# Kernel optimization log

Hardware: AMD Instinct MI355X
Metric: run time of the kernel (lower is better)

## Reference

```python
import jax, jax.numpy as jnp
import numpy as np

USER_NUM = 500000
ITEM_NUM = 100000
D = 256        # embedding_size
MEM = 32       # memory_size
ATT = 256      # attention_size
B = 4096       # batch
NF = 64        # friends per user (padded with index == USER_NUM)


def _u(k, shape):
    return jax.random.uniform(k, shape, dtype=jnp.float32, minval=-0.1, maxval=0.1)


def setup_inputs() -> dict:
    key = jax.random.key(0)
    ks = jax.random.split(key, 12)
    return {
        "input_u": jax.random.randint(ks[0], (B,), 0, USER_NUM + 1),
        "input_i": jax.random.randint(ks[1], (B,), 0, ITEM_NUM),
        "input_uf": jax.random.randint(ks[2], (B, NF), 0, USER_NUM + 1),
        "uidW": _u(ks[3], (USER_NUM + 1, D)),
        "iidW": _u(ks[4], (ITEM_NUM, D)),
        "i_bias": jnp.zeros((ITEM_NUM,), jnp.float32),
        "Key": _u(ks[5], (D, MEM)),
        "Mem": jnp.ones((MEM, D), jnp.float32),
        "WA": _u(ks[6], (D, ATT)),
        "BA": jnp.zeros((ATT,), jnp.float32),
        "U_omega": _u(ks[7], (ATT, 1)),
        "att_exp1": jax.random.normal(ks[8], (2 * D, 2), jnp.float32) * 0.05,
    }


def _l2norm(x, axis):
    # torch F.normalize(p=2): x / max(||x||, eps)
    n = jnp.sqrt(jnp.sum(x * x, axis=axis, keepdims=True))
    return x / jnp.maximum(n, 1e-12)


def reference(input_u, input_i, input_uf, uidW, iidW, i_bias, Key, Mem, WA, BA, U_omega, att_exp1):
    uid = uidW[input_u]                        # [B, D]
    iid = iidW[input_i]                        # [B, D]
    i_b = i_bias[input_i]                      # [B]
    fe = uidW[input_uf]                        # [B, F, D]
    frien_num = (input_uf != USER_NUM).astype(jnp.float32)  # [B, F] valid mask
    fe = frien_num[:, :, None] * fe

    uid_n = _l2norm(uid, axis=1)
    fe_n = _l2norm(fe, axis=2)
    cross = uid_n[:, None, :] * fe_n           # [B, F, D]

    att_key = jnp.einsum('bfd,dm->bfm', cross, Key)          # [B, F, M]
    att_mem = jax.nn.softmax(att_key, axis=0)                # NOTE: softmax over BATCH dim (faithful)
    att_mem = frien_num[:, :, None] * att_mem

    f1 = jnp.einsum('bfm,md->bfd', att_mem, Mem)             # [B, F, D]
    f2 = f1 * fe                                             # [B, F, D]

    h = jax.nn.relu(jnp.einsum('bfd,da->bfa', f2, WA) + BA)  # [B, F, A]
    j = jnp.exp(jnp.einsum('bfa,ao->bfo', h, U_omega))       # [B, F, 1]
    j = frien_num[:, :, None] * j
    w = j / (jnp.sum(j, axis=1, keepdims=True) + 1e-8)       # [B, F, 1]
    friend = jnp.sum(w * f2, axis=1)                         # [B, D]
    # dropout(p=dp) in eval mode -> identity

    user = uid + friend
    att1 = jax.nn.softmax(jnp.concatenate([uid, user], axis=1) @ att_exp1, axis=1)  # [B, 2]
    user_f = uid * att1[:, 0:1] + user * att1[:, 1:2]
    score = jnp.sum(user_f * iid, axis=1) + i_b              # [B]
    return score
```

## Files before the change

kernel.cpp:

```cpp
#include <hip/hip_runtime.h>

#define USER_NUM 500000
#define BATCH 4096
#define NF 64
#define DIM 256
#define MEMN 32
#define ATTN 256

typedef short bf16x8 __attribute__((ext_vector_type(8)));
typedef float f32x4 __attribute__((ext_vector_type(4)));

__device__ __forceinline__ unsigned short f2bf(float f) {
    unsigned u = __float_as_uint(f);
    u += 0x7FFFu + ((u >> 16) & 1u);
    return (unsigned short)(u >> 16);
}
__device__ __forceinline__ float bf2f(unsigned short s) {
    return __uint_as_float(((unsigned)s) << 16);
}

__device__ __forceinline__ float block_reduce_sum(float v, float* scr) {
#pragma unroll
    for (int o = 32; o; o >>= 1) v += __shfl_xor(v, o, 64);
    __syncthreads();
    if ((threadIdx.x & 63) == 0) scr[threadIdx.x >> 6] = v;
    __syncthreads();
    return scr[0] + scr[1] + scr[2] + scr[3];
}

#define WS_AK    0u
#define WS_KEYT  33554432u
#define WS_MEMT  33570816u
#define WS_WATT  33587200u
#define WS_PART  33718272u
#define WS_SSUM  33783808u

__global__ __launch_bounds__(256) void kprep(const float* __restrict__ Key,
                                             const float* __restrict__ Mem,
                                             const float* __restrict__ WA,
                                             unsigned short* __restrict__ keyT,
                                             unsigned short* __restrict__ memT,
                                             unsigned short* __restrict__ watt) {
    int gid = blockIdx.x * 256 + threadIdx.x;
    if (gid < 8192) {
        int m = gid >> 8, d = gid & 255;
        keyT[gid] = f2bf(Key[d * 32 + m]);
    } else if (gid < 16384) {
        int e = gid - 8192, d = e >> 5, m = e & 31;
        memT[e] = f2bf(Mem[m * 256 + d]);
    } else {
        int e = gid - 16384;
        int kt = e >> 13, r = e & 8191, a = r >> 5, kk = r & 31;
        watt[e] = f2bf(WA[(kt * 32 + kk) * 256 + a]);
    }
}

__global__ __launch_bounds__(256) void katt(const int* __restrict__ input_u,
                                            const int* __restrict__ input_uf,
                                            const float* __restrict__ uidW,
                                            const unsigned short* __restrict__ keyT_ws,
                                            float* __restrict__ ak) {
    extern __shared__ char smem[];
    float* uidn = (float*)(smem + 50688);
    float* scr  = (float*)(smem + 51712);
    const int b = blockIdx.x, t = threadIdx.x;
    const int w = t >> 6, l = t & 63;

    {
        const uint4* src = (const uint4*)keyT_ws;
#pragma unroll
        for (int k = 0; k < 4; k++) {
            int ci = t + 256 * k;
            int m = ci >> 5, c = ci & 31;
            *(uint4*)(smem + 33792 + m * 528 + c * 16) = src[ci];
        }
    }
    int iu = input_u[b];
    float uv = uidW[(size_t)iu * DIM + t];
    float ss = block_reduce_sum(uv * uv, scr);
    float inv = 1.0f / fmaxf(sqrtf(ss), 1e-12f);
    uidn[t] = uv * inv;
    __syncthreads();

    float4 un4 = *(const float4*)(uidn + l * 4);
    for (int i = 0; i < 16; i++) {
        int f = w * 16 + i;
        int idx = input_uf[b * NF + f];
        float mk = (idx != USER_NUM) ? 1.0f : 0.0f;
        float4 fe = ((const float4*)(uidW + (size_t)idx * DIM))[l];
        fe.x *= mk; fe.y *= mk; fe.z *= mk; fe.w *= mk;
        float s2 = fe.x * fe.x + fe.y * fe.y + fe.z * fe.z + fe.w * fe.w;
#pragma unroll
        for (int o = 32; o; o >>= 1) s2 += __shfl_xor(s2, o, 64);
        float rn = 1.0f / fmaxf(sqrtf(s2), 1e-12f);
        ushort4 o4;
        o4.x = f2bf(un4.x * fe.x * rn);
        o4.y = f2bf(un4.y * fe.y * rn);
        o4.z = f2bf(un4.z * fe.z * rn);
        o4.w = f2bf(un4.w * fe.w * rn);
        *(ushort4*)(smem + f * 528 + l * 8) = o4;
    }
    __syncthreads();

    bf16x8 aF[8];
#pragma unroll
    for (int k = 0; k < 8; k++)
        aF[k] = *(const bf16x8*)(smem + (w * 16 + (l & 15)) * 528 + k * 64 + (l >> 4) * 16);
#pragma unroll
    for (int mt = 0; mt < 2; mt++) {
        f32x4 acc = {0.f, 0.f, 0.f, 0.f};
#pragma unroll
        for (int k = 0; k < 8; k++) {
            bf16x8 bF = *(const bf16x8*)(smem + 33792 + (mt * 16 + (l & 15)) * 528 + k * 64 + (l >> 4) * 16);
            acc = __builtin_amdgcn_mfma_f32_16x16x32_bf16(aF[k], bF, acc, 0, 0, 0);
        }
        int m = mt * 16 + (l & 15);
        int fbase = w * 16 + (l >> 4) * 4;
#pragma unroll
        for (int r = 0; r < 4; r++)
            ak[((size_t)b * NF + fbase + r) * MEMN + m] = acc[r];
    }
}

__global__ __launch_bounds__(256) void ksum1(const float* __restrict__ ak, float* __restrict__ part) {
    __shared__ float pl[256];
    int bid = blockIdx.x;
    int f = bid >> 3, c = bid & 7;
    int t = threadIdx.x, m = t & 31, g = t >> 5;
    float s = 0.f;
    size_t base = ((size_t)(c * 512 + g) * NF + f) * MEMN + m;
    for (int i = 0; i < 64; i++) {
        s += __expf(ak[base]);
        base += (size_t)8 * NF * MEMN;
    }
    pl[t] = s;
    __syncthreads();
    if (t < 32) {
        float tot = 0.f;
#pragma unroll
        for (int gg = 0; gg < 8; gg++) tot += pl[gg * 32 + t];
        part[c * 2048 + f * 32 + t] = tot;
    }
}
__global__ __launch_bounds__(256) void ksum2(const float* __restrict__ part, float* __restrict__ ssum) {
    int fm = blockIdx.x * 256 + threadIdx.x;
    float s = 0.f;
#pragma unroll
    for (int c = 0; c < 8; c++) s += part[c * 2048 + fm];
    ssum[fm] = s;
}

#define OFF_AM   33792
#define OFF_MEMT 38912
#define OFF_WAT  33792
#define OFF_JP   59392
#define OFF_W    60416
#define OFF_UF   60672
#define OFF_MSK  60928
#define OFF_SCR  61184
__global__ __launch_bounds__(256) void kmain(const int* __restrict__ input_u,
                                             const int* __restrict__ input_i,
                                             const int* __restrict__ input_uf,
                                             const float* __restrict__ uidW,
                                             const float* __restrict__ iidW,
                                             const float* __restrict__ i_bias,
                                             const float* __restrict__ BA,
                                             const float* __restrict__ U_omega,
                                             const float* __restrict__ att_exp1,
                                             const float* __restrict__ ak,
                                             const float* __restrict__ ssum_ws,
                                             const unsigned short* __restrict__ memT_ws,
                                             const unsigned short* __restrict__ watt_ws,
                                             float* __restrict__ out) {
    extern __shared__ char smem[];
    float* jpL  = (float*)(smem + OFF_JP);
    float* wL   = (float*)(smem + OFF_W);
    int*   ufL  = (int*)(smem + OFF_UF);
    float* mskL = (float*)(smem + OFF_MSK);
    float* scr  = (float*)(smem + OFF_SCR);
    const int b = blockIdx.x, t = threadIdx.x;
    const int w = t >> 6, l = t & 63;

    int iu = input_u[b], ii = input_i[b];
    float uidv = uidW[(size_t)iu * DIM + t];
    float iidv = iidW[(size_t)ii * DIM + t];
    float ib   = i_bias[ii];
    float ae00 = att_exp1[t * 2], ae01 = att_exp1[t * 2 + 1];
    float ae10 = att_exp1[(DIM + t) * 2], ae11 = att_exp1[(DIM + t) * 2 + 1];

    if (t < 64) {
        int uf = input_uf[b * NF + t];
        ufL[t] = uf;
        mskL[t] = (uf != USER_NUM) ? 1.0f : 0.0f;
    }
    {
        const uint4* src = (const uint4*)memT_ws;
#pragma unroll
        for (int k = 0; k < 4; k++) {
            int ci = t + 256 * k;
            int d = ci >> 2, c = ci & 3;
            *(uint4*)(smem + OFF_MEMT + d * 80 + c * 16) = src[ci];
        }
    }
    __syncthreads();

    {
        const float4* akp = (const float4*)(ak + (size_t)b * 2048);
        const float4* sp  = (const float4*)ssum_ws;
        float4 a0 = akp[2 * t], a1 = akp[2 * t + 1];
        float4 s0 = sp[2 * t],  s1 = sp[2 * t + 1];
        float mk = mskL[t >> 2];
        float v0 = mk * __expf(a0.x) / s0.x;
        float v1 = mk * __expf(a0.y) / s0.y;
        float v2 = mk * __expf(a0.z) / s0.z;
        float v3 = mk * __expf(a0.w) / s0.w;
        float v4 = mk * __expf(a1.x) / s1.x;
        float v5 = mk * __expf(a1.y) / s1.y;
        float v6 = mk * __expf(a1.z) / s1.z;
        float v7 = mk * __expf(a1.w) / s1.w;
        uint4 pk;
        pk.x = (unsigned)f2bf(v0) | ((unsigned)f2bf(v1) << 16);
        pk.y = (unsigned)f2bf(v2) | ((unsigned)f2bf(v3) << 16);
        pk.z = (unsigned)f2bf(v4) | ((unsigned)f2bf(v5) << 16);
        pk.w = (unsigned)f2bf(v6) | ((unsigned)f2bf(v7) << 16);
        *(uint4*)(smem + OFF_AM + (t >> 2) * 80 + (t & 3) * 16) = pk;
    }
    __syncthreads();

    {
        bf16x8 aF[4];
#pragma unroll
        for (int ft = 0; ft < 4; ft++)
            aF[ft] = *(const bf16x8*)(smem + OFF_AM + (ft * 16 + (l & 15)) * 80 + (l >> 4) * 16);
#pragma unroll
        for (int dti = 0; dti < 4; dti++) {
            int dt = 4 * w + dti;
            bf16x8 bF = *(const bf16x8*)(smem + OFF_MEMT + (dt * 16 + (l & 15)) * 80 + (l >> 4) * 16);
            int dcol = dt * 16 + (l & 15);
#pragma unroll
            for (int ft = 0; ft < 4; ft++) {
                f32x4 acc = {0.f, 0.f, 0.f, 0.f};
                acc = __builtin_amdgcn_mfma_f32_16x16x32_bf16(aF[ft], bF, acc, 0, 0, 0);
                int fbase = ft * 16 + (l >> 4) * 4;
#pragma unroll
                for (int r = 0; r < 4; r++)
                    *(unsigned short*)(smem + (fbase + r) * 528 + dcol * 2) = f2bf(acc[r]);
            }
        }
    }
    __syncthreads();

    for (int i = 0; i < 16; i++) {
        int f = w * 16 + i;
        int idx = ufL[f];
        float mk = mskL[f];
        float4 fe = ((const float4*)(uidW + (size_t)idx * DIM))[l];
        ushort4* p = (ushort4*)(smem + f * 528 + l * 8);
        ushort4 q = *p;
        ushort4 o4;
        o4.x = f2bf(bf2f(q.x) * fe.x * mk);
        o4.y = f2bf(bf2f(q.y) * fe.y * mk);
        o4.z = f2bf(bf2f(q.z) * fe.z * mk);
        o4.w = f2bf(bf2f(q.w) * fe.w * mk);
        *p = o4;
    }
    __syncthreads();

    f32x4 acc[4][4];
    {
        f32x4 z = {0.f, 0.f, 0.f, 0.f};
#pragma unroll
        for (int ft = 0; ft < 4; ft++)
#pragma unroll
            for (int at = 0; at < 4; at++) acc[ft][at] = z;
    }
    for (int kt = 0; kt < 8; kt++) {
        const uint4* src = ((const uint4*)watt_ws) + kt * 1024;
#pragma unroll
        for (int k = 0; k < 4; k++) {
            int ci = t + 256 * k;
            int a = ci >> 2, c = ci & 3;
            *(uint4*)(smem + OFF_WAT + a * 80 + c * 16) = src[ci];
        }
        __syncthreads();
        bf16x8 aF[4], bF[4];
#pragma unroll
        for (int ft = 0; ft < 4; ft++)
            aF[ft] = *(const bf16x8*)(smem + (ft * 16 + (l & 15)) * 528 + kt * 64 + (l >> 4) * 16);
#pragma unroll
        for (int at = 0; at < 4; at++)
            bF[at] = *(const bf16x8*)(smem + OFF_WAT + (64 * w + at * 16 + (l & 15)) * 80 + (l >> 4) * 16);
#pragma unroll
        for (int ft = 0; ft < 4; ft++)
#pragma unroll
            for (int at = 0; at < 4; at++)
                acc[ft][at] = __builtin_amdgcn_mfma_f32_16x16x32_bf16(aF[ft], bF[at], acc[ft][at], 0, 0, 0);
        __syncthreads();
    }
    {
        float jp[16];
#pragma unroll
        for (int i = 0; i < 16; i++) jp[i] = 0.f;
#pragma unroll
        for (int at = 0; at < 4; at++) {
            int a = 64 * w + at * 16 + (l & 15);
            float ba = BA[a], uw = U_omega[a];
#pragma unroll
            for (int ft = 0; ft < 4; ft++)
#pragma unroll
                for (int r = 0; r < 4; r++) {
                    float h = fmaxf(acc[ft][at][r] + ba, 0.f);
                    jp[ft * 4 + r] += h * uw;
                }
        }
#pragma unroll
        for (int mask = 1; mask < 16; mask <<= 1)
#pragma unroll
            for (int i = 0; i < 16; i++) jp[i] += __shfl_xor(jp[i], mask, 64);
        if ((l & 15) == 0) {
#pragma unroll
            for (int ft = 0; ft < 4; ft++)
#pragma unroll
                for (int r = 0; r < 4; r++)
                    jpL[w * 64 + ft * 16 + (l >> 4) * 4 + r] = jp[ft * 4 + r];
        }
    }
    __syncthreads();

    if (t < 64) {
        float logit = jpL[t] + jpL[64 + t] + jpL[128 + t] + jpL[192 + t];
        float jv = mskL[t] * __expf(logit);
        float s = jv;
#pragma unroll
        for (int o = 32; o; o >>= 1) s += __shfl_xor(s, o, 64);
        wL[t] = jv / (s + 1e-8f);
    }
    __syncthreads();

    float fr = 0.f;
#pragma unroll 8
    for (int f = 0; f < 64; f++)
        fr += wL[f] * bf2f(*(unsigned short*)(smem + f * 528 + t * 2));

    float user = uidv + fr;
    float l0 = block_reduce_sum(uidv * ae00 + user * ae10, scr);
    float l1 = block_reduce_sum(uidv * ae01 + user * ae11, scr);
    float mx = fmaxf(l0, l1);
    float e0 = __expf(l0 - mx), e1 = __expf(l1 - mx);
    float rinv = 1.0f / (e0 + e1);
    float a0w = e0 * rinv, a1w = e1 * rinv;
    float sc = block_reduce_sum((uidv * a0w + user * a1w) * iidv, scr);
    if (t == 0) out[b] = sc + ib;
}

extern "C" void kernel_launch(void* const* d_in, const int* in_sizes, int n_in,
                              void* d_out, int out_size, void* d_ws, size_t ws_size,
                              hipStream_t stream) {
    const int*   input_u  = (const int*)d_in[0];
    const int*   input_i  = (const int*)d_in[1];
    const int*   input_uf = (const int*)d_in[2];
    const float* uidW     = (const float*)d_in[3];
    const float* iidW     = (const float*)d_in[4];
    const float* i_bias   = (const float*)d_in[5];
    const float* Key      = (const float*)d_in[6];
    const float* Mem      = (const float*)d_in[7];
    const float* WA       = (const float*)d_in[8];
    const float* BA       = (const float*)d_in[9];
    const float* U_omega  = (const float*)d_in[10];
    const float* att_exp1 = (const float*)d_in[11];
    float* out = (float*)d_out;
    char* ws = (char*)d_ws;

    float*          ak   = (float*)(ws + WS_AK);
    unsigned short* keyT = (unsigned short*)(ws + WS_KEYT);
    unsigned short* memT = (unsigned short*)(ws + WS_MEMT);
    unsigned short* watt = (unsigned short*)(ws + WS_WATT);
    float*          part = (float*)(ws + WS_PART);
    float*          ssum = (float*)(ws + WS_SSUM);

    hipLaunchKernelGGL(kprep, dim3(320), dim3(256), 0, stream, Key, Mem, WA, keyT, memT, watt);
    hipLaunchKernelGGL(katt, dim3(BATCH), dim3(256), 51776, stream, input_u, input_uf, uidW, keyT, ak);
    hipLaunchKernelGGL(ksum1, dim3(512), dim3(256), 0, stream, ak, part);
    hipLaunchKernelGGL(ksum2, dim3(8), dim3(256), 0, stream, part, ssum);
    hipLaunchKernelGGL(kmain, dim3(BATCH), dim3(256), 61440, stream, input_u, input_i, input_uf,
                       uidW, iidW, i_bias, BA, U_omega, att_exp1, ak, ssum, memT, watt, out);
}
```

Before: 908.2 us.

## Cache masked friend embeddings as bf16 and read weight fragments from global

katt now writes the masked friend embeddings as bf16 to a workspace buffer, and kmain reads them back contiguously instead of re-gathering the random uidW rows. Key, Mem and WA fragments are loaded straight from global/L2 into MFMA operands rather than staged through LDS, which removes the per-k-tile syncthreads in kmain and shrinks shared memory. Gathers are batched into register arrays for more memory-level parallelism, and launch bounds request higher occupancy. In exchange it adds 128MB of workspace traffic, rounds fe to bf16 before the f2 product, and puts more register pressure on the kernels.

```diff
diff --git a/kernel.cpp b/kernel.cpp
--- a/kernel.cpp
+++ b/kernel.cpp
@@ -18,6 +18,9 @@
 __device__ __forceinline__ float bf2f(unsigned short s) {
     return __uint_as_float(((unsigned)s) << 16);
 }
+__device__ __forceinline__ bf16x8 as_frag(uint4 v) {
+    return __builtin_bit_cast(bf16x8, v);
+}
 
 __device__ __forceinline__ float block_reduce_sum(float v, float* scr) {
 #pragma unroll
@@ -29,11 +32,12 @@
 }
 
 #define WS_AK    0u
-#define WS_KEYT  33554432u
-#define WS_MEMT  33570816u
-#define WS_WATT  33587200u
-#define WS_PART  33718272u
-#define WS_SSUM  33783808u
+#define WS_FE    33554432u
+#define WS_KEYT  167772160u
+#define WS_MEMT  167788544u
+#define WS_WATT  167804928u
+#define WS_PART  167936000u
+#define WS_SSUM  168001536u
 
 __global__ __launch_bounds__(256) void kprep(const float* __restrict__ Key,
                                              const float* __restrict__ Mem,
@@ -55,25 +59,24 @@
     }
 }
 
-__global__ __launch_bounds__(256) void katt(const int* __restrict__ input_u,
-                                            const int* __restrict__ input_uf,
-                                            const float* __restrict__ uidW,
-                                            const unsigned short* __restrict__ keyT_ws,
-                                            float* __restrict__ ak) {
+__global__ __launch_bounds__(256, 4) void katt(const int* __restrict__ input_u,
+                                               const int* __restrict__ input_uf,
+                                               const float* __restrict__ uidW,
+                                               const unsigned short* __restrict__ keyT_ws,
+                                               unsigned short* __restrict__ fe_ws,
+                                               float* __restrict__ ak) {
     extern __shared__ char smem[];
-    float* uidn = (float*)(smem + 50688);
-    float* scr  = (float*)(smem + 51712);
+    float* uidn = (float*)(smem + 33792);
+    float* scr  = (float*)(smem + 34816);
+    int*   ufL  = (int*)(smem + 34880);
+    float* mskL = (float*)(smem + 35136);
     const int b = blockIdx.x, t = threadIdx.x;
-    const int w = t >> 6, l = t & 63;
-
-    {
-        const uint4* src = (const uint4*)keyT_ws;
-#pragma unroll
-        for (int k = 0; k < 4; k++) {
-            int ci = t + 256 * k;
-            int m = ci >> 5, c = ci & 31;
-            *(uint4*)(smem + 33792 + m * 528 + c * 16) = src[ci];
-        }
+    const int w = t >> 6, l = t & 63, q = l >> 4;
+
+    if (t < 64) {
+        int uf = input_uf[b * NF + t];
+        ufL[t] = uf;
+        mskL[t] = (uf != USER_NUM) ? 1.0f : 0.0f;
     }
     int iu = input_u[b];
     float uv = uidW[(size_t)iu * DIM + t];
@@ -83,42 +86,51 @@
     __syncthreads();
 
     float4 un4 = *(const float4*)(uidn + l * 4);
+    float4 fe[16];
+#pragma unroll
+    for (int i = 0; i < 16; i++) {
+        int idx = ufL[w * 16 + i];
+        fe[i] = ((const float4*)(uidW + (size_t)idx * DIM))[l];
+    }
+#pragma unroll
     for (int i = 0; i < 16; i++) {
         int f = w * 16 + i;
-        int idx = input_uf[b * NF + f];
-        float mk = (idx != USER_NUM) ? 1.0f : 0.0f;
-        float4 fe = ((const float4*)(uidW + (size_t)idx * DIM))[l];
-        fe.x *= mk; fe.y *= mk; fe.z *= mk; fe.w *= mk;
-        float s2 = fe.x * fe.x + fe.y * fe.y + fe.z * fe.z + fe.w * fe.w;
+        float mk = mskL[f];
+        float x = fe[i].x * mk, y = fe[i].y * mk, z = fe[i].z * mk, ww = fe[i].w * mk;
+        float s2 = x * x + y * y + z * z + ww * ww;
 #pragma unroll
         for (int o = 32; o; o >>= 1) s2 += __shfl_xor(s2, o, 64);
         float rn = 1.0f / fmaxf(sqrtf(s2), 1e-12f);
+        ushort4 fb;
+        fb.x = f2bf(x); fb.y = f2bf(y); fb.z = f2bf(z); fb.w = f2bf(ww);
+        *(ushort4*)(fe_ws + (size_t)b * 16384 + f * 256 + l * 4) = fb;
         ushort4 o4;
-        o4.x = f2bf(un4.x * fe.x * rn);
-        o4.y = f2bf(un4.y * fe.y * rn);
-        o4.z = f2bf(un4.z * fe.z * rn);
-        o4.w = f2bf(un4.w * fe.w * rn);
+        o4.x = f2bf(un4.x * x * rn);
+        o4.y = f2bf(un4.y * y * rn);
+        o4.z = f2bf(un4.z * z * rn);
+        o4.w = f2bf(un4.w * ww * rn);
         *(ushort4*)(smem + f * 528 + l * 8) = o4;
     }
     __syncthreads();
 
-    bf16x8 aF[8];
-#pragma unroll
-    for (int k = 0; k < 8; k++)
-        aF[k] = *(const bf16x8*)(smem + (w * 16 + (l & 15)) * 528 + k * 64 + (l >> 4) * 16);
-#pragma unroll
-    for (int mt = 0; mt < 2; mt++) {
-        f32x4 acc = {0.f, 0.f, 0.f, 0.f};
-#pragma unroll
-        for (int k = 0; k < 8; k++) {
-            bf16x8 bF = *(const bf16x8*)(smem + 33792 + (mt * 16 + (l & 15)) * 528 + k * 64 + (l >> 4) * 16);
-            acc = __builtin_amdgcn_mfma_f32_16x16x32_bf16(aF[k], bF, acc, 0, 0, 0);
-        }
-        int m = mt * 16 + (l & 15);
-        int fbase = w * 16 + (l >> 4) * 4;
-#pragma unroll
-        for (int r = 0; r < 4; r++)
-            ak[((size_t)b * NF + fbase + r) * MEMN + m] = acc[r];
+    const uint4* kp = (const uint4*)keyT_ws;
+    f32x4 acc0 = {0.f, 0.f, 0.f, 0.f}, acc1 = {0.f, 0.f, 0.f, 0.f};
+#pragma unroll
+    for (int kt = 0; kt < 8; kt++) {
+        bf16x8 aF = *(const bf16x8*)(smem + (w * 16 + (l & 15)) * 528 + kt * 64 + q * 16);
+        bf16x8 b0 = as_frag(kp[(l & 15) * 32 + kt * 4 + q]);
+        bf16x8 b1 = as_frag(kp[((l & 15) + 16) * 32 + kt * 4 + q]);
+        acc0 = __builtin_amdgcn_mfma_f32_16x16x32_bf16(aF, b0, acc0, 0, 0, 0);
+        acc1 = __builtin_amdgcn_mfma_f32_16x16x32_bf16(aF, b1, acc1, 0, 0, 0);
+    }
+    {
+        int fbase = w * 16 + q * 4;
+        int m = l & 15;
+#pragma unroll
+        for (int r = 0; r < 4; r++) {
+            ak[((size_t)b * NF + fbase + r) * MEMN + m]      = acc0[r];
+            ak[((size_t)b * NF + fbase + r) * MEMN + 16 + m] = acc1[r];
+        }
     }
 }
 
@@ -151,35 +163,32 @@
 }
 
 #define OFF_AM   33792
-#define OFF_MEMT 38912
-#define OFF_WAT  33792
-#define OFF_JP   59392
-#define OFF_W    60416
-#define OFF_UF   60672
-#define OFF_MSK  60928
-#define OFF_SCR  61184
-__global__ __launch_bounds__(256) void kmain(const int* __restrict__ input_u,
-                                             const int* __restrict__ input_i,
-                                             const int* __restrict__ input_uf,
-                                             const float* __restrict__ uidW,
-                                             const float* __restrict__ iidW,
-                                             const float* __restrict__ i_bias,
-                                             const float* __restrict__ BA,
-                                             const float* __restrict__ U_omega,
-                                             const float* __restrict__ att_exp1,
-                                             const float* __restrict__ ak,
-                                             const float* __restrict__ ssum_ws,
-                                             const unsigned short* __restrict__ memT_ws,
-                                             const unsigned short* __restrict__ watt_ws,
-                                             float* __restrict__ out) {
+#define OFF_JP   38912
+#define OFF_W    39936
+#define OFF_MSK  40448
+#define OFF_SCR  40704
+__global__ __launch_bounds__(256, 3) void kmain(const int* __restrict__ input_u,
+                                                const int* __restrict__ input_i,
+                                                const int* __restrict__ input_uf,
+                                                const float* __restrict__ uidW,
+                                                const float* __restrict__ iidW,
+                                                const float* __restrict__ i_bias,
+                                                const float* __restrict__ BA,
+                                                const float* __restrict__ U_omega,
+                                                const float* __restrict__ att_exp1,
+                                                const float* __restrict__ ak,
+                                                const float* __restrict__ ssum_ws,
+                                                const unsigned short* __restrict__ fe_ws,
+                                                const unsigned short* __restrict__ memT_ws,
+                                                const unsigned short* __restrict__ watt_ws,
+                                                float* __restrict__ out) {
     extern __shared__ char smem[];
     float* jpL  = (float*)(smem + OFF_JP);
     float* wL   = (float*)(smem + OFF_W);
-    int*   ufL  = (int*)(smem + OFF_UF);
     float* mskL = (float*)(smem + OFF_MSK);
     float* scr  = (float*)(smem + OFF_SCR);
     const int b = blockIdx.x, t = threadIdx.x;
-    const int w = t >> 6, l = t & 63;
+    const int w = t >> 6, l = t & 63, q = l >> 4;
 
     int iu = input_u[b], ii = input_i[b];
     float uidv = uidW[(size_t)iu * DIM + t];
@@ -190,17 +199,7 @@
 
     if (t < 64) {
         int uf = input_uf[b * NF + t];
-        ufL[t] = uf;
         mskL[t] = (uf != USER_NUM) ? 1.0f : 0.0f;
-    }
-    {
-        const uint4* src = (const uint4*)memT_ws;
-#pragma unroll
-        for (int k = 0; k < 4; k++) {
-            int ci = t + 256 * k;
-            int d = ci >> 2, c = ci & 3;
-            *(uint4*)(smem + OFF_MEMT + d * 80 + c * 16) = src[ci];
-        }
     }
     __syncthreads();
 
@@ -228,20 +227,21 @@
     __syncthreads();
 
     {
+        const uint4* mp = (const uint4*)memT_ws;
         bf16x8 aF[4];
 #pragma unroll
         for (int ft = 0; ft < 4; ft++)
-            aF[ft] = *(const bf16x8*)(smem + OFF_AM + (ft * 16 + (l & 15)) * 80 + (l >> 4) * 16);
+            aF[ft] = *(const bf16x8*)(smem + OFF_AM + (ft * 16 + (l & 15)) * 80 + q * 16);
 #pragma unroll
         for (int dti = 0; dti < 4; dti++) {
             int dt = 4 * w + dti;
-            bf16x8 bF = *(const bf16x8*)(smem + OFF_MEMT + (dt * 16 + (l & 15)) * 80 + (l >> 4) * 16);
+            bf16x8 bF = as_frag(mp[(dt * 16 + (l & 15)) * 4 + q]);
             int dcol = dt * 16 + (l & 15);
 #pragma unroll
             for (int ft = 0; ft < 4; ft++) {
                 f32x4 acc = {0.f, 0.f, 0.f, 0.f};
                 acc = __builtin_amdgcn_mfma_f32_16x16x32_bf16(aF[ft], bF, acc, 0, 0, 0);
-                int fbase = ft * 16 + (l >> 4) * 4;
+                int fbase = ft * 16 + q * 4;
 #pragma unroll
                 for (int r = 0; r < 4; r++)
                     *(unsigned short*)(smem + (fbase + r) * 528 + dcol * 2) = f2bf(acc[r]);
@@ -250,19 +250,25 @@
     }
     __syncthreads();
 
-    for (int i = 0; i < 16; i++) {
-        int f = w * 16 + i;
-        int idx = ufL[f];
-        float mk = mskL[f];
-        float4 fe = ((const float4*)(uidW + (size_t)idx * DIM))[l];
-        ushort4* p = (ushort4*)(smem + f * 528 + l * 8);
-        ushort4 q = *p;
-        ushort4 o4;
-        o4.x = f2bf(bf2f(q.x) * fe.x * mk);
-        o4.y = f2bf(bf2f(q.y) * fe.y * mk);
-        o4.z = f2bf(bf2f(q.z) * fe.z * mk);
-        o4.w = f2bf(bf2f(q.w) * fe.w * mk);
-        *p = o4;
+    {
+        ushort4 feb[16];
+#pragma unroll
+        for (int i = 0; i < 16; i++) {
+            int f = w * 16 + i;
+            feb[i] = *(const ushort4*)(fe_ws + (size_t)b * 16384 + f * 256 + l * 4);
+        }
+#pragma unroll
+        for (int i = 0; i < 16; i++) {
+            int f = w * 16 + i;
+            ushort4* p = (ushort4*)(smem + f * 528 + l * 8);
+            ushort4 fv = *p;
+            ushort4 o4;
+            o4.x = f2bf(bf2f(fv.x) * bf2f(feb[i].x));
+            o4.y = f2bf(bf2f(fv.y) * bf2f(feb[i].y));
+            o4.z = f2bf(bf2f(fv.z) * bf2f(feb[i].z));
+            o4.w = f2bf(bf2f(fv.w) * bf2f(feb[i].w));
+            *p = o4;
+        }
     }
     __syncthreads();
 
@@ -274,28 +280,22 @@
 #pragma unroll
             for (int at = 0; at < 4; at++) acc[ft][at] = z;
     }
-    for (int kt = 0; kt < 8; kt++) {
-        const uint4* src = ((const uint4*)watt_ws) + kt * 1024;
-#pragma unroll
-        for (int k = 0; k < 4; k++) {
-            int ci = t + 256 * k;
-            int a = ci >> 2, c = ci & 3;
-            *(uint4*)(smem + OFF_WAT + a * 80 + c * 16) = src[ci];
-        }
-        __syncthreads();
-        bf16x8 aF[4], bF[4];
-#pragma unroll
-        for (int ft = 0; ft < 4; ft++)
-            aF[ft] = *(const bf16x8*)(smem + (ft * 16 + (l & 15)) * 528 + kt * 64 + (l >> 4) * 16);
-#pragma unroll
-        for (int at = 0; at < 4; at++)
-            bF[at] = *(const bf16x8*)(smem + OFF_WAT + (64 * w + at * 16 + (l & 15)) * 80 + (l >> 4) * 16);
-#pragma unroll
-        for (int ft = 0; ft < 4; ft++)
+    {
+        const uint4* wp = (const uint4*)watt_ws;
+        for (int kt = 0; kt < 8; kt++) {
+            bf16x8 aF[4], bF[4];
+#pragma unroll
+            for (int ft = 0; ft < 4; ft++)
+                aF[ft] = *(const bf16x8*)(smem + (ft * 16 + (l & 15)) * 528 + kt * 64 + q * 16);
 #pragma unroll
             for (int at = 0; at < 4; at++)
-                acc[ft][at] = __builtin_amdgcn_mfma_f32_16x16x32_bf16(aF[ft], bF[at], acc[ft][at], 0, 0, 0);
-        __syncthreads();
+                bF[at] = as_frag(wp[kt * 1024 + (64 * w + at * 16 + (l & 15)) * 4 + q]);
+#pragma unroll
+            for (int ft = 0; ft < 4; ft++)
+#pragma unroll
+                for (int at = 0; at < 4; at++)
+                    acc[ft][at] = __builtin_amdgcn_mfma_f32_16x16x32_bf16(aF[ft], bF[at], acc[ft][at], 0, 0, 0);
+        }
     }
     {
         float jp[16];
@@ -322,7 +322,7 @@
             for (int ft = 0; ft < 4; ft++)
 #pragma unroll
                 for (int r = 0; r < 4; r++)
-                    jpL[w * 64 + ft * 16 + (l >> 4) * 4 + r] = jp[ft * 4 + r];
+                    jpL[w * 64 + ft * 16 + q * 4 + r] = jp[ft * 4 + r];
         }
     }
     __syncthreads();
@@ -372,6 +372,7 @@
     char* ws = (char*)d_ws;
 
     float*          ak   = (float*)(ws + WS_AK);
+    unsigned short* fe   = (unsigned short*)(ws + WS_FE);
     unsigned short* keyT = (unsigned short*)(ws + WS_KEYT);
     unsigned short* memT = (unsigned short*)(ws + WS_MEMT);
     unsigned short* watt = (unsigned short*)(ws + WS_WATT);
@@ -379,9 +380,9 @@
     float*          ssum = (float*)(ws + WS_SSUM);
 
     hipLaunchKernelGGL(kprep, dim3(320), dim3(256), 0, stream, Key, Mem, WA, keyT, memT, watt);
-    hipLaunchKernelGGL(katt, dim3(BATCH), dim3(256), 51776, stream, input_u, input_uf, uidW, keyT, ak);
+    hipLaunchKernelGGL(katt, dim3(BATCH), dim3(256), 35392, stream, input_u, input_uf, uidW, keyT, fe, ak);
     hipLaunchKernelGGL(ksum1, dim3(512), dim3(256), 0, stream, ak, part);
     hipLaunchKernelGGL(ksum2, dim3(8), dim3(256), 0, stream, part, ssum);
-    hipLaunchKernelGGL(kmain, dim3(BATCH), dim3(256), 61440, stream, input_u, input_i, input_uf,
-                       uidW, iidW, i_bias, BA, U_omega, att_exp1, ak, ssum, memT, watt, out);
-}
+    hipLaunchKernelGGL(kmain, dim3(BATCH), dim3(256), 40768, stream, input_u, input_i, input_uf,
+                       uidW, iidW, i_bias, BA, U_omega, att_exp1, ak, ssum, fe, memT, watt, out);
+}
```

After: 802.0 us. 1.13x faster.
